# Kernel optimization log

Measured on AMD Instinct MI355X. Metric: run time of the kernel, lower is better.

The kernel has to match this reference:

```python
import jax, jax.numpy as jnp
import numpy as np

B, L, D = 4, 4096, 1024

def setup_inputs() -> dict:
    key = jax.random.key(0)
    k1, k2, k3 = jax.random.split(key, 3)
    limit = float(np.sqrt(6.0 / (D + D)))  # glorot_uniform
    return {
        "x": jax.random.normal(k1, (B, L, D), dtype=jnp.float32),
        "state": jnp.zeros((B, D), dtype=jnp.float32),
        "erase_kernel": jax.random.uniform(k2, (D, D), minval=-limit, maxval=limit, dtype=jnp.float32),
        "erase_bias": jnp.zeros((D,), dtype=jnp.float32),
        "write_kernel": jax.random.uniform(k3, (D, D), minval=-limit, maxval=limit, dtype=jnp.float32),
        "write_bias": jnp.zeros((D,), dtype=jnp.float32),
    }

def reference(x, state, erase_kernel, erase_bias, write_kernel, write_bias):
    x = x.astype(jnp.float32)
    # Gates: [B, L, D]
    erase = jax.nn.sigmoid(jnp.einsum('bld,de->ble', x, erase_kernel) + erase_bias)
    write = jax.nn.sigmoid(jnp.einsum('bld,de->ble', x, write_kernel) + write_bias)

    def step(s, inp):
        e_t, w_t, x_t = inp  # each [B, D]
        s = s * (1.0 - e_t) + w_t * x_t
        return s, s

    # scan over time axis
    _, outs = jax.lax.scan(
        step, state,
        (jnp.swapaxes(erase, 0, 1), jnp.swapaxes(write, 0, 1), jnp.swapaxes(x, 0, 1)),
    )  # outs: [L, B, D]
    return jnp.swapaxes(outs, 0, 1)  # [B, L, D]
```

## Files before the change

### kernel.cpp

```cpp
#include <hip/hip_runtime.h>
#include <stdint.h>

#define MB (1ull << 20)

typedef __attribute__((ext_vector_type(8))) short bf16x8;
typedef __attribute__((ext_vector_type(8))) unsigned short u16x8;
typedef __attribute__((ext_vector_type(4))) float f32x4;

static __device__ __forceinline__ unsigned short f2bf(float f) {
    unsigned u = __builtin_bit_cast(unsigned, f);
    u += 0x7fffu + ((u >> 16) & 1u);
    return (unsigned short)(u >> 16);
}
static __device__ __forceinline__ float bf2f(unsigned u16) {
    return __builtin_bit_cast(float, u16 << 16);
}

#define GLDS(gp, lp) __builtin_amdgcn_global_load_lds(                                   \
        (const __attribute__((address_space(1))) void*)(gp),                             \
        (__attribute__((address_space(3))) void*)(lp), 16, 0, 0)

__global__ __launch_bounds__(256) void cvt_x_kernel(const float* __restrict__ x,
                                                    unsigned short* __restrict__ xb, int n8) {
    int i = blockIdx.x * blockDim.x + threadIdx.x;
    if (i >= n8) return;
    const float4* px = (const float4*)x + (size_t)i * 2;
    float4 a = px[0], b = px[1];
    u16x8 o;
    o[0] = f2bf(a.x); o[1] = f2bf(a.y); o[2] = f2bf(a.z); o[3] = f2bf(a.w);
    o[4] = f2bf(b.x); o[5] = f2bf(b.y); o[6] = f2bf(b.z); o[7] = f2bf(b.w);
    ((u16x8*)xb)[i] = o;
}

__global__ __launch_bounds__(256) void cvt_w_kernel(const float* __restrict__ ek,
                                                    const float* __restrict__ wk,
                                                    unsigned short* __restrict__ wt) {
    int t = blockIdx.x * blockDim.x + threadIdx.x;
    int n = t >> 7;
    int kb = (t & 127) * 8;
    const float* src = (n < 1024) ? ek : wk;
    int col = n & 1023;
    u16x8 o;
#pragma unroll
    for (int j = 0; j < 8; ++j) o[j] = f2bf(src[(size_t)(kb + j) * 1024 + col]);
    ((u16x8*)wt)[t] = o;
}

__global__ __launch_bounds__(512, 2) void gate_gemm(const unsigned short* __restrict__ Xb,
                                                    const unsigned short* __restrict__ Wt,
                                                    const float* __restrict__ eb,
                                                    const float* __restrict__ wb,
                                                    const float* __restrict__ xf,
                                                    unsigned short* __restrict__ Ag,
                                                    unsigned short* __restrict__ WXg) {
    __shared__ alignas(16) unsigned short As[4][256 * 32];
    __shared__ alignas(16) unsigned short Bs[4][256 * 32];
    const int tid = threadIdx.x;
    const int lane = tid & 63;
    const int w = tid >> 6;
    const int wm = w >> 2, wn = w & 3;
    const int colq = lane & 15, rowq = lane >> 4;

    const int orig = blockIdx.y * 64 + blockIdx.x;
    const int swz = (orig & 7) * 64 + (orig >> 3);
    const int m0 = (swz & 63) * 256;
    const int n0g = (swz >> 6) * 256;

    const int srow = tid >> 2;
    const int ksrc = (((tid & 3) ^ ((tid >> 3) & 3)) * 8);
    const int aslot = ((rowq ^ ((colq >> 1) & 3)) * 8);

    f32x4 acc[8][4] = {};

    auto stage = [&](int ts) {
        const int bi = ts & 3;
        const int k0 = (ts < 32 ? ts : 31) * 32;
        const unsigned short* sa = Xb + (size_t)(m0 + srow) * 1024 + k0 + ksrc;
        const unsigned short* sb = Wt + (size_t)(n0g + srow) * 1024 + k0 + ksrc;
        unsigned short* la = &As[bi][tid * 8];
        unsigned short* lb = &Bs[bi][tid * 8];
        GLDS(sa, la);
        GLDS(sa + 128 * 1024, la + 4096);
        GLDS(sb, lb);
        GLDS(sb + 128 * 1024, lb + 4096);
    };

    stage(0); stage(1); stage(2);

    for (int t = 0; t < 32; ++t) {
        stage(t + 3);
        asm volatile("s_waitcnt vmcnt(12)" ::: "memory");
        __builtin_amdgcn_s_barrier();
        asm volatile("" ::: "memory");

        const int bi = t & 3;
        bf16x8 af[8], bfr[4];
#pragma unroll
        for (int f = 0; f < 8; ++f)
            af[f] = *(const bf16x8*)&As[bi][(wm * 128 + f * 16 + colq) * 32 + aslot];
#pragma unroll
        for (int f = 0; f < 4; ++f)
            bfr[f] = *(const bf16x8*)&Bs[bi][(wn * 64 + f * 16 + colq) * 32 + aslot];

        __builtin_amdgcn_s_setprio(1);
#pragma unroll
        for (int i2 = 0; i2 < 8; ++i2)
#pragma unroll
            for (int j2 = 0; j2 < 4; ++j2)
                acc[i2][j2] = __builtin_amdgcn_mfma_f32_16x16x32_bf16(af[i2], bfr[j2], acc[i2][j2], 0, 0, 0);
        __builtin_amdgcn_s_setprio(0);
        asm volatile("" ::: "memory");
        __builtin_amdgcn_s_barrier();
    }

    const bool isE = (n0g < 1024);
    const float* bias = isE ? eb : wb;
    const int nb = isE ? n0g : (n0g - 1024);
    unsigned short* outp = isE ? Ag : WXg;
#pragma unroll
    for (int j2 = 0; j2 < 4; ++j2) {
        const int gn = nb + wn * 64 + j2 * 16 + colq;
        const float bv = bias[gn];
#pragma unroll
        for (int i2 = 0; i2 < 8; ++i2) {
            const int gm = m0 + wm * 128 + i2 * 16 + rowq * 4;
#pragma unroll
            for (int r = 0; r < 4; ++r) {
                const size_t oidx = (size_t)(gm + r) * 1024 + gn;
                const float z = acc[i2][j2][r] + bv;
                float val;
                if (isE) val = 1.0f / (1.0f + __expf(z));
                else     val = (1.0f / (1.0f + __expf(-z))) * xf[oidx];
                outp[oidx] = f2bf(val);
            }
        }
    }
}

__global__ __launch_bounds__(256) void scan_phase1(const unsigned short* __restrict__ Ag,
                                                   const unsigned short* __restrict__ WXg,
                                                   float* __restrict__ Asum, float* __restrict__ Bsum) {
    const int c = blockIdx.x, b = blockIdx.y, dz = blockIdx.z;
    const int d2 = dz * 256 + threadIdx.x;
    size_t base = ((size_t)(b * 4096 + c * 64)) * 512 + d2;
    const unsigned* A2 = (const unsigned*)Ag;
    const unsigned* W2 = (const unsigned*)WXg;
    float ap0 = 1.f, ap1 = 1.f, s0 = 0.f, s1 = 0.f;
#pragma unroll 8
    for (int i = 0; i < 64; ++i) {
        unsigned ua = A2[base], uw = W2[base];
        float a0 = bf2f(ua & 0xffffu), a1 = bf2f(ua >> 16);
        float w0 = bf2f(uw & 0xffffu), w1 = bf2f(uw >> 16);
        s0 = fmaf(s0, a0, w0);
        s1 = fmaf(s1, a1, w1);
        ap0 *= a0;
        ap1 *= a1;
        base += 512;
    }
    const size_t so = ((size_t)(b * 64 + c)) * 512 + d2;
    ((float2*)Asum)[so] = make_float2(ap0, ap1);
    ((float2*)Bsum)[so] = make_float2(s0, s1);
}

__global__ __launch_bounds__(256) void scan_phase2(const float* __restrict__ st,
                                                   const float* __restrict__ Asum,
                                                   const float* __restrict__ Bsum,
                                                   float* __restrict__ Sin) {
    const int t = blockIdx.x * 256 + threadIdx.x;
    const int b = t >> 10, d = t & 1023;
    float s = st[t];
    size_t idx = (size_t)(b * 64) * 1024 + d;
#pragma unroll 8
    for (int c = 0; c < 64; ++c) {
        Sin[idx] = s;
        s = fmaf(s, Asum[idx], Bsum[idx]);
        idx += 1024;
    }
}

__global__ __launch_bounds__(256) void scan_phase3(const unsigned short* __restrict__ Ag,
                                                   const unsigned short* __restrict__ WXg,
                                                   const float* __restrict__ Sin,
                                                   float* __restrict__ out) {
    const int c = blockIdx.x, b = blockIdx.y, dz = blockIdx.z;
    const int d2 = dz * 256 + threadIdx.x;
    size_t base = ((size_t)(b * 4096 + c * 64)) * 512 + d2;
    const unsigned* A2 = (const unsigned*)Ag;
    const unsigned* W2 = (const unsigned*)WXg;
    float2 sv = ((const float2*)Sin)[((size_t)(b * 64 + c)) * 512 + d2];
    float s0 = sv.x, s1 = sv.y;
    float2* o2 = (float2*)out;
#pragma unroll 4
    for (int i = 0; i < 64; ++i) {
        unsigned ua = A2[base], uw = W2[base];
        s0 = fmaf(s0, bf2f(ua & 0xffffu), bf2f(uw & 0xffffu));
        s1 = fmaf(s1, bf2f(ua >> 16), bf2f(uw >> 16));
        o2[base] = make_float2(s0, s1);
        base += 512;
    }
}

extern "C" void kernel_launch(void* const* d_in, const int* in_sizes, int n_in,
                              void* d_out, int out_size, void* d_ws, size_t ws_size,
                              hipStream_t stream) {
    const float* x  = (const float*)d_in[0];
    const float* st = (const float*)d_in[1];
    const float* ek = (const float*)d_in[2];
    const float* eb = (const float*)d_in[3];
    const float* wk = (const float*)d_in[4];
    const float* wb = (const float*)d_in[5];
    float* out = (float*)d_out;
    char* ws = (char*)d_ws;

    unsigned short* xb = (unsigned short*)ws;
    unsigned short* wt = (unsigned short*)(ws + 32 * MB);
    unsigned short* Ag = (unsigned short*)(ws + 36 * MB);
    unsigned short* WXg = (unsigned short*)(ws + 68 * MB);
    float* Asum = (float*)(ws + 100 * MB);
    float* Bsum = Asum + (size_t)4 * 64 * 1024;
    float* Sin  = Bsum + (size_t)4 * 64 * 1024;

    cvt_x_kernel<<<8192, 256, 0, stream>>>(x, xb, 2097152);
    cvt_w_kernel<<<1024, 256, 0, stream>>>(ek, wk, wt);

    dim3 ggrid(64, 8);
    gate_gemm<<<ggrid, 512, 0, stream>>>(xb, wt, eb, wb, x, Ag, WXg);

    dim3 sgrid(64, 4, 2);
    scan_phase1<<<sgrid, 256, 0, stream>>>(Ag, WXg, Asum, Bsum);
    scan_phase2<<<16, 256, 0, stream>>>(st, Asum, Bsum, Sin);
    scan_phase3<<<sgrid, 256, 0, stream>>>(Ag, WXg, Sin, out);
}
```

Before: 351.4 us.

## Restructure gate GEMM with K=64 double-buffered stages, LDS epilogue, wider scan loads

```diff
diff --git a/kernel.cpp b/kernel.cpp
--- a/kernel.cpp
+++ b/kernel.cpp
@@ -19,6 +19,12 @@
 #define GLDS(gp, lp) __builtin_amdgcn_global_load_lds(                                   \
         (const __attribute__((address_space(1))) void*)(gp),                             \
         (__attribute__((address_space(3))) void*)(lp), 16, 0, 0)
+
+static __device__ __forceinline__ void wg_barrier() {
+    asm volatile("" ::: "memory");
+    __builtin_amdgcn_s_barrier();
+    asm volatile("" ::: "memory");
+}
 
 __global__ __launch_bounds__(256) void cvt_x_kernel(const float* __restrict__ x,
                                                     unsigned short* __restrict__ xb, int n8) {
@@ -50,89 +56,179 @@
                                                     const unsigned short* __restrict__ Wt,
                                                     const float* __restrict__ eb,
                                                     const float* __restrict__ wb,
-                                                    const float* __restrict__ xf,
                                                     unsigned short* __restrict__ Ag,
                                                     unsigned short* __restrict__ WXg) {
-    __shared__ alignas(16) unsigned short As[4][256 * 32];
-    __shared__ alignas(16) unsigned short Bs[4][256 * 32];
+    __shared__ alignas(16) unsigned short S[65536];
     const int tid = threadIdx.x;
-    const int lane = tid & 63;
-    const int w = tid >> 6;
+    const int lane = tid & 63, w = tid >> 6;
     const int wm = w >> 2, wn = w & 3;
     const int colq = lane & 15, rowq = lane >> 4;
 
-    const int orig = blockIdx.y * 64 + blockIdx.x;
+    const int orig = blockIdx.x;
     const int swz = (orig & 7) * 64 + (orig >> 3);
     const int m0 = (swz & 63) * 256;
     const int n0g = (swz >> 6) * 256;
 
-    const int srow = tid >> 2;
-    const int ksrc = (((tid & 3) ^ ((tid >> 3) & 3)) * 8);
-    const int aslot = ((rowq ^ ((colq >> 1) & 3)) * 8);
+    uint soff[8], ldso[8];
+#pragma unroll
+    for (int l = 0; l < 8; ++l) {
+        const int o = (l & 3) * 512 + tid;
+        const int half = o >> 10;
+        const int r = (o >> 3) & 127;
+        const int slot = o & 7;
+        const int c = slot ^ (r & 7);
+        const int grow = ((l < 4) ? m0 : n0g) + half * 128 + r;
+        soff[l] = (uint)grow * 1024u + (uint)c * 8u;
+        ldso[l] = (uint)((l < 4 ? 0 : 32768) + half * 8192 + r * 64 + slot * 8);
+    }
+
+    auto stage = [&](int s) {
+        const int k0 = (s < 16 ? s : 15) * 64;
+        const int db = (s & 1) * 16384;
+#pragma unroll
+        for (int l = 0; l < 8; ++l) {
+            const unsigned short* g = ((l < 4) ? Xb : Wt) + soff[l] + k0;
+            GLDS(g, &S[db + ldso[l]]);
+        }
+    };
+
+    const int axk = colq & 7;
+    const int abase = wm * 8192 + colq * 64;
+    const int bbase = 32768 + (wn >> 1) * 8192 + ((wn & 1) * 64 + colq) * 64;
 
     f32x4 acc[8][4] = {};
-
-    auto stage = [&](int ts) {
-        const int bi = ts & 3;
-        const int k0 = (ts < 32 ? ts : 31) * 32;
-        const unsigned short* sa = Xb + (size_t)(m0 + srow) * 1024 + k0 + ksrc;
-        const unsigned short* sb = Wt + (size_t)(n0g + srow) * 1024 + k0 + ksrc;
-        unsigned short* la = &As[bi][tid * 8];
-        unsigned short* lb = &Bs[bi][tid * 8];
-        GLDS(sa, la);
-        GLDS(sa + 128 * 1024, la + 4096);
-        GLDS(sb, lb);
-        GLDS(sb + 128 * 1024, lb + 4096);
-    };
-
-    stage(0); stage(1); stage(2);
-
-    for (int t = 0; t < 32; ++t) {
-        stage(t + 3);
-        asm volatile("s_waitcnt vmcnt(12)" ::: "memory");
-        __builtin_amdgcn_s_barrier();
-        asm volatile("" ::: "memory");
-
-        const int bi = t & 3;
-        bf16x8 af[8], bfr[4];
-#pragma unroll
-        for (int f = 0; f < 8; ++f)
-            af[f] = *(const bf16x8*)&As[bi][(wm * 128 + f * 16 + colq) * 32 + aslot];
-#pragma unroll
-        for (int f = 0; f < 4; ++f)
-            bfr[f] = *(const bf16x8*)&Bs[bi][(wn * 64 + f * 16 + colq) * 32 + aslot];
-
+    bf16x8 af[4][2], bfr[2][2];
+
+    stage(0);
+
+    for (int s = 0; s < 16; ++s) {
+        const int db = (s & 1) * 16384;
+        stage(s + 1);
+        asm volatile("s_waitcnt vmcnt(8)" ::: "memory");
+        wg_barrier();
+#pragma unroll
+        for (int i = 0; i < 4; ++i)
+#pragma unroll
+            for (int ks = 0; ks < 2; ++ks)
+                af[i][ks] = *(const bf16x8*)&S[db + abase + i * 1024 + (((ks * 4 + rowq) ^ axk) * 8)];
+#pragma unroll
+        for (int j = 0; j < 2; ++j)
+#pragma unroll
+            for (int ks = 0; ks < 2; ++ks)
+                bfr[j][ks] = *(const bf16x8*)&S[db + bbase + j * 1024 + (((ks * 4 + rowq) ^ axk) * 8)];
         __builtin_amdgcn_s_setprio(1);
 #pragma unroll
-        for (int i2 = 0; i2 < 8; ++i2)
-#pragma unroll
-            for (int j2 = 0; j2 < 4; ++j2)
-                acc[i2][j2] = __builtin_amdgcn_mfma_f32_16x16x32_bf16(af[i2], bfr[j2], acc[i2][j2], 0, 0, 0);
+        for (int i = 0; i < 4; ++i)
+#pragma unroll
+            for (int j = 0; j < 2; ++j)
+#pragma unroll
+                for (int ks = 0; ks < 2; ++ks)
+                    acc[i][j] = __builtin_amdgcn_mfma_f32_16x16x32_bf16(af[i][ks], bfr[j][ks], acc[i][j], 0, 0, 0);
         __builtin_amdgcn_s_setprio(0);
-        asm volatile("" ::: "memory");
-        __builtin_amdgcn_s_barrier();
+        wg_barrier();
+
+#pragma unroll
+        for (int j = 0; j < 2; ++j)
+#pragma unroll
+            for (int ks = 0; ks < 2; ++ks)
+                bfr[j][ks] = *(const bf16x8*)&S[db + bbase + (2 + j) * 1024 + (((ks * 4 + rowq) ^ axk) * 8)];
+        wg_barrier();
+        __builtin_amdgcn_s_setprio(1);
+#pragma unroll
+        for (int i = 0; i < 4; ++i)
+#pragma unroll
+            for (int j = 0; j < 2; ++j)
+#pragma unroll
+                for (int ks = 0; ks < 2; ++ks)
+                    acc[i][2 + j] = __builtin_amdgcn_mfma_f32_16x16x32_bf16(af[i][ks], bfr[j][ks], acc[i][2 + j], 0, 0, 0);
+        __builtin_amdgcn_s_setprio(0);
+        wg_barrier();
+
+#pragma unroll
+        for (int i = 0; i < 4; ++i)
+#pragma unroll
+            for (int ks = 0; ks < 2; ++ks)
+                af[i][ks] = *(const bf16x8*)&S[db + abase + (4 + i) * 1024 + (((ks * 4 + rowq) ^ axk) * 8)];
+        wg_barrier();
+        __builtin_amdgcn_s_setprio(1);
+#pragma unroll
+        for (int i = 0; i < 4; ++i)
+#pragma unroll
+            for (int j = 0; j < 2; ++j)
+#pragma unroll
+                for (int ks = 0; ks < 2; ++ks)
+                    acc[4 + i][2 + j] = __builtin_amdgcn_mfma_f32_16x16x32_bf16(af[i][ks], bfr[j][ks], acc[4 + i][2 + j], 0, 0, 0);
+        __builtin_amdgcn_s_setprio(0);
+        wg_barrier();
+
+#pragma unroll
+        for (int j = 0; j < 2; ++j)
+#pragma unroll
+            for (int ks = 0; ks < 2; ++ks)
+                bfr[j][ks] = *(const bf16x8*)&S[db + bbase + j * 1024 + (((ks * 4 + rowq) ^ axk) * 8)];
+        wg_barrier();
+        __builtin_amdgcn_s_setprio(1);
+#pragma unroll
+        for (int i = 0; i < 4; ++i)
+#pragma unroll
+            for (int j = 0; j < 2; ++j)
+#pragma unroll
+                for (int ks = 0; ks < 2; ++ks)
+                    acc[4 + i][j] = __builtin_amdgcn_mfma_f32_16x16x32_bf16(af[i][ks], bfr[j][ks], acc[4 + i][j], 0, 0, 0);
+        __builtin_amdgcn_s_setprio(0);
+        wg_barrier();
     }
 
     const bool isE = (n0g < 1024);
     const float* bias = isE ? eb : wb;
     const int nb = isE ? n0g : (n0g - 1024);
     unsigned short* outp = isE ? Ag : WXg;
-#pragma unroll
-    for (int j2 = 0; j2 < 4; ++j2) {
-        const int gn = nb + wn * 64 + j2 * 16 + colq;
-        const float bv = bias[gn];
-#pragma unroll
-        for (int i2 = 0; i2 < 8; ++i2) {
-            const int gm = m0 + wm * 128 + i2 * 16 + rowq * 4;
-#pragma unroll
-            for (int r = 0; r < 4; ++r) {
-                const size_t oidx = (size_t)(gm + r) * 1024 + gn;
-                const float z = acc[i2][j2][r] + bv;
-                float val;
-                if (isE) val = 1.0f / (1.0f + __expf(z));
-                else     val = (1.0f / (1.0f + __expf(-z))) * xf[oidx];
-                outp[oidx] = f2bf(val);
+    float bv[4];
+#pragma unroll
+    for (int j = 0; j < 4; ++j) bv[j] = bias[nb + wn * 64 + j * 16 + colq];
+
+    float* Ep = (float*)S;
+    const int wbase = w * 4096;
+    const int rl = lane >> 3;
+    const int c0 = (lane & 7) * 8;
+
+#pragma unroll
+    for (int ih = 0; ih < 2; ++ih) {
+        __syncthreads();
+#pragma unroll
+        for (int i = 0; i < 4; ++i)
+#pragma unroll
+            for (int j = 0; j < 4; ++j)
+#pragma unroll
+                for (int r = 0; r < 4; ++r) {
+                    const int r2 = i * 16 + rowq * 4 + r;
+                    const int cc = (j * 16 + colq) ^ (rowq * 16);
+                    const float z = acc[ih * 4 + i][j][r] + bv[j];
+                    Ep[wbase + r2 * 64 + cc] = 1.0f / (1.0f + __expf(isE ? z : -z));
+                }
+        __syncthreads();
+#pragma unroll
+        for (int it = 0; it < 8; ++it) {
+            const int rr = it * 8 + rl;
+            const int key = ((rr >> 2) & 3) * 16;
+            const int cx = c0 ^ key;
+            f32x4 v0 = *(const f32x4*)&Ep[wbase + rr * 64 + cx];
+            f32x4 v1 = *(const f32x4*)&Ep[wbase + rr * 64 + cx + 4];
+            const int grow = m0 + wm * 128 + ih * 64 + rr;
+            const size_t oidx = (size_t)grow * 1024 + (nb + wn * 64 + c0);
+            u16x8 ov;
+            if (isE) {
+                ov[0] = f2bf(v0[0]); ov[1] = f2bf(v0[1]); ov[2] = f2bf(v0[2]); ov[3] = f2bf(v0[3]);
+                ov[4] = f2bf(v1[0]); ov[5] = f2bf(v1[1]); ov[6] = f2bf(v1[2]); ov[7] = f2bf(v1[3]);
+            } else {
+                u16x8 xv = *(const u16x8*)&Xb[oidx];
+#pragma unroll
+                for (int q = 0; q < 4; ++q) {
+                    ov[q]     = f2bf(v0[q] * bf2f((unsigned)(unsigned short)xv[q]));
+                    ov[4 + q] = f2bf(v1[q] * bf2f((unsigned)(unsigned short)xv[4 + q]));
+                }
             }
+            *(u16x8*)&outp[oidx] = ov;
         }
     }
 }
@@ -140,26 +236,27 @@
 __global__ __launch_bounds__(256) void scan_phase1(const unsigned short* __restrict__ Ag,
                                                    const unsigned short* __restrict__ WXg,
                                                    float* __restrict__ Asum, float* __restrict__ Bsum) {
-    const int c = blockIdx.x, b = blockIdx.y, dz = blockIdx.z;
-    const int d2 = dz * 256 + threadIdx.x;
-    size_t base = ((size_t)(b * 4096 + c * 64)) * 512 + d2;
-    const unsigned* A2 = (const unsigned*)Ag;
-    const unsigned* W2 = (const unsigned*)WXg;
-    float ap0 = 1.f, ap1 = 1.f, s0 = 0.f, s1 = 0.f;
+    const int c = blockIdx.x, b = blockIdx.y;
+    const int d4 = threadIdx.x;
+    size_t base = ((size_t)(b * 4096 + c * 64)) * 256 + d4;
+    const uint2* A2 = (const uint2*)Ag;
+    const uint2* W2 = (const uint2*)WXg;
+    float ap[4] = {1.f, 1.f, 1.f, 1.f}, sv[4] = {0.f, 0.f, 0.f, 0.f};
 #pragma unroll 8
     for (int i = 0; i < 64; ++i) {
-        unsigned ua = A2[base], uw = W2[base];
-        float a0 = bf2f(ua & 0xffffu), a1 = bf2f(ua >> 16);
-        float w0 = bf2f(uw & 0xffffu), w1 = bf2f(uw >> 16);
-        s0 = fmaf(s0, a0, w0);
-        s1 = fmaf(s1, a1, w1);
-        ap0 *= a0;
-        ap1 *= a1;
-        base += 512;
-    }
-    const size_t so = ((size_t)(b * 64 + c)) * 512 + d2;
-    ((float2*)Asum)[so] = make_float2(ap0, ap1);
-    ((float2*)Bsum)[so] = make_float2(s0, s1);
+        uint2 ua = A2[base], uw = W2[base];
+        float a0 = bf2f(ua.x & 0xffffu), a1 = bf2f(ua.x >> 16);
+        float a2 = bf2f(ua.y & 0xffffu), a3 = bf2f(ua.y >> 16);
+        float w0 = bf2f(uw.x & 0xffffu), w1 = bf2f(uw.x >> 16);
+        float w2 = bf2f(uw.y & 0xffffu), w3 = bf2f(uw.y >> 16);
+        sv[0] = fmaf(sv[0], a0, w0); sv[1] = fmaf(sv[1], a1, w1);
+        sv[2] = fmaf(sv[2], a2, w2); sv[3] = fmaf(sv[3], a3, w3);
+        ap[0] *= a0; ap[1] *= a1; ap[2] *= a2; ap[3] *= a3;
+        base += 256;
+    }
+    const size_t so = ((size_t)(b * 64 + c)) * 256 + d4;
+    ((float4*)Asum)[so] = make_float4(ap[0], ap[1], ap[2], ap[3]);
+    ((float4*)Bsum)[so] = make_float4(sv[0], sv[1], sv[2], sv[3]);
 }
 
 __global__ __launch_bounds__(256) void scan_phase2(const float* __restrict__ st,
@@ -182,21 +279,23 @@
                                                    const unsigned short* __restrict__ WXg,
                                                    const float* __restrict__ Sin,
                                                    float* __restrict__ out) {
-    const int c = blockIdx.x, b = blockIdx.y, dz = blockIdx.z;
-    const int d2 = dz * 256 + threadIdx.x;
-    size_t base = ((size_t)(b * 4096 + c * 64)) * 512 + d2;
-    const unsigned* A2 = (const unsigned*)Ag;
-    const unsigned* W2 = (const unsigned*)WXg;
-    float2 sv = ((const float2*)Sin)[((size_t)(b * 64 + c)) * 512 + d2];
-    float s0 = sv.x, s1 = sv.y;
-    float2* o2 = (float2*)out;
+    const int c = blockIdx.x, b = blockIdx.y;
+    const int d4 = threadIdx.x;
+    size_t base = ((size_t)(b * 4096 + c * 64)) * 256 + d4;
+    const uint2* A2 = (const uint2*)Ag;
+    const uint2* W2 = (const uint2*)WXg;
+    float4 svv = ((const float4*)Sin)[((size_t)(b * 64 + c)) * 256 + d4];
+    float s0 = svv.x, s1 = svv.y, s2 = svv.z, s3 = svv.w;
+    float4* o4 = (float4*)out;
 #pragma unroll 4
     for (int i = 0; i < 64; ++i) {
-        unsigned ua = A2[base], uw = W2[base];
-        s0 = fmaf(s0, bf2f(ua & 0xffffu), bf2f(uw & 0xffffu));
-        s1 = fmaf(s1, bf2f(ua >> 16), bf2f(uw >> 16));
-        o2[base] = make_float2(s0, s1);
-        base += 512;
+        uint2 ua = A2[base], uw = W2[base];
+        s0 = fmaf(s0, bf2f(ua.x & 0xffffu), bf2f(uw.x & 0xffffu));
+        s1 = fmaf(s1, bf2f(ua.x >> 16),     bf2f(uw.x >> 16));
+        s2 = fmaf(s2, bf2f(ua.y & 0xffffu), bf2f(uw.y & 0xffffu));
+        s3 = fmaf(s3, bf2f(ua.y >> 16),     bf2f(uw.y >> 16));
+        o4[base] = make_float4(s0, s1, s2, s3);
+        base += 256;
     }
 }
 
@@ -223,10 +322,9 @@
     cvt_x_kernel<<<8192, 256, 0, stream>>>(x, xb, 2097152);
     cvt_w_kernel<<<1024, 256, 0, stream>>>(ek, wk, wt);
 
-    dim3 ggrid(64, 8);
-    gate_gemm<<<ggrid, 512, 0, stream>>>(xb, wt, eb, wb, x, Ag, WXg);
-
-    dim3 sgrid(64, 4, 2);
+    gate_gemm<<<512, 512, 0, stream>>>(xb, wt, eb, wb, Ag, WXg);
+
+    dim3 sgrid(64, 4);
     scan_phase1<<<sgrid, 256, 0, stream>>>(Ag, WXg, Asum, Bsum);
     scan_phase2<<<16, 256, 0, stream>>>(st, Asum, Bsum, Sin);
     scan_phase3<<<sgrid, 256, 0, stream>>>(Ag, WXg, Sin, out);
```

Result: faster. 290.1 us (-17.5%).
